# Kernel tuning notes

Measured on AMD Instinct MI355X. Metric: run time of the kernel, lower is better.

Reference implementation:

```python
import jax, jax.numpy as jnp
import numpy as np

N = 100000   # nodes
E = 1000000  # edges
F = 64       # in_features == out_features
ALPHA = 0.2  # leaky-relu negative slope


def setup_inputs() -> dict:
    key = jax.random.key(0)
    k = jax.random.split(key, 6)
    h = jax.random.normal(k[0], (N, F), jnp.float32)
    W = jax.random.normal(k[1], (F, F), jnp.float32) * 0.1   # Linear weight [out,in]
    Wb = jnp.zeros((F,), jnp.float32)
    a = jax.random.normal(k[2], (2 * F,), jnp.float32) * 0.1  # attn vector (Linear(2F,1))
    ab = jnp.zeros((), jnp.float32)
    src = jax.random.randint(k[3], (E,), 0, N, dtype=jnp.int32)
    dst = jax.random.randint(k[4], (E,), 0, N, dtype=jnp.int32)
    return {"h": h, "W": W, "Wb": Wb, "a": a, "ab": ab, "src": src, "dst": dst}


def reference(h, W, Wb, a, ab, src, dst):
    # Wh = W(h)  (dropout is identity in eval mode / dropout=0)
    Wh = h @ W.T + Wb                                   # [N, F]
    # e = leakyrelu(a([Wh_src || Wh_dst])) ; split a to avoid concat
    a_src, a_dst = a[:F], a[F:]
    e = jax.nn.leaky_relu(Wh[src] @ a_src + Wh[dst] @ a_dst + ab, ALPHA)  # [E]
    # segment softmax over destination nodes (DGL mailbox softmax)
    m = jax.ops.segment_max(e, dst, num_segments=N)     # [N], -inf for empty
    m = jnp.where(jnp.isfinite(m), m, 0.0)
    ex = jnp.exp(e - m[dst])                            # [E]
    denom = jax.ops.segment_sum(ex, dst, num_segments=N)
    attn = ex / jnp.where(denom[dst] > 0, denom[dst], 1.0)
    # weighted scatter-sum of source features to destinations
    h_prime = jax.ops.segment_sum(attn[:, None] * Wh[src], dst, num_segments=N)  # [N, F]
    return h_prime
```

## Files before the change

### kernel.cpp

```cpp
#include <hip/hip_runtime.h>

#define NF 64
#define ALPHA 0.2f
#define BSH 7
#define BNODES 128
#define CAPG 2048
#define PB 4096
#define HB 800
#define NBIN 1024

typedef unsigned int  uint;
typedef unsigned short ushort;

typedef __attribute__((ext_vector_type(8))) short  short8;
typedef __attribute__((ext_vector_type(4))) float  floatx4;

__device__ __forceinline__ ushort f2bf(float x) {
    uint u = __float_as_uint(x);
    u += 0x7fffu + ((u >> 16) & 1u);
    return (ushort)(u >> 16);
}

__device__ __forceinline__ short8 pack8(float4 lo, float4 hi) {
    short8 r;
    r[0] = (short)f2bf(lo.x); r[1] = (short)f2bf(lo.y);
    r[2] = (short)f2bf(lo.z); r[3] = (short)f2bf(lo.w);
    r[4] = (short)f2bf(hi.x); r[5] = (short)f2bf(hi.y);
    r[6] = (short)f2bf(hi.z); r[7] = (short)f2bf(hi.w);
    return r;
}

__global__ __launch_bounds__(256) void wh_part_kernel(
    const float* __restrict__ h, const float* __restrict__ W,
    const float* __restrict__ Wb, const float* __restrict__ a,
    ushort* __restrict__ whbf, float* __restrict__ s_src, float* __restrict__ s_dst,
    const int* __restrict__ src, const int* __restrict__ dst,
    int* __restrict__ bctr, uint* __restrict__ tmp,
    int N, int E, int edgeB, int NB)
{
    __shared__ uint   stage[PB];
    __shared__ ushort bid[PB];
    __shared__ int    hist[HB];
    __shared__ int    lbase[HB];
    __shared__ int    ctr[HB];
    __shared__ int    gbase[HB];
    __shared__ int    sw[256];

    int t = threadIdx.x;

    if ((int)blockIdx.x < edgeB) {
        int base = (int)blockIdx.x * PB;
        int total = E - base; if (total > PB) total = PB; if (total < 0) total = 0;

        for (int i = t; i < HB; i += 256) hist[i] = 0;
        __syncthreads();

        uint pk[16]; int bb[16];
        #pragma unroll
        for (int g = 0; g < 4; ++g) {
            int ei = base + g * 1024 + t * 4;
            int s4[4], d4[4];
            if (ei + 3 < E) {
                int4 sv = *(const int4*)&src[ei];
                int4 dv = *(const int4*)&dst[ei];
                s4[0]=sv.x; s4[1]=sv.y; s4[2]=sv.z; s4[3]=sv.w;
                d4[0]=dv.x; d4[1]=dv.y; d4[2]=dv.z; d4[3]=dv.w;
            } else {
                #pragma unroll
                for (int j = 0; j < 4; ++j) {
                    int e = ei + j;
                    s4[j] = (e < E) ? src[e] : -1;
                    d4[j] = (e < E) ? dst[e] : -1;
                }
            }
            #pragma unroll
            for (int j = 0; j < 4; ++j) {
                int i16 = g * 4 + j;
                if (d4[j] >= 0) {
                    pk[i16] = ((uint)s4[j] << BSH) | (uint)(d4[j] & (BNODES - 1));
                    bb[i16] = d4[j] >> BSH;
                    atomicAdd(&hist[bb[i16]], 1);
                } else bb[i16] = -1;
            }
        }
        __syncthreads();

        int b0 = t * 4;
        int c0 = 0, c1 = 0, c2 = 0, c3 = 0;
        if (b0 < HB)     c0 = hist[b0];
        if (b0 + 1 < HB) c1 = hist[b0+1];
        if (b0 + 2 < HB) c2 = hist[b0+2];
        if (b0 + 3 < HB) c3 = hist[b0+3];
        int tsum = c0 + c1 + c2 + c3;
        sw[t] = tsum; __syncthreads();
        for (int off = 1; off < 256; off <<= 1) {
            int x = (t >= off) ? sw[t - off] : 0;
            __syncthreads();
            sw[t] += x;
            __syncthreads();
        }
        int ex = sw[t] - tsum;
        if (b0 < HB)     { lbase[b0]   = ex; ex += c0; }
        if (b0 + 1 < HB) { lbase[b0+1] = ex; ex += c1; }
        if (b0 + 2 < HB) { lbase[b0+2] = ex; ex += c2; }
        if (b0 + 3 < HB) { lbase[b0+3] = ex; }
        __syncthreads();

        for (int q = t; q < NB; q += 256) {
            int c = hist[q];
            gbase[q] = c ? atomicAdd(&bctr[q], c) : 0;
            ctr[q] = lbase[q];
        }
        __syncthreads();

        #pragma unroll
        for (int i = 0; i < 16; ++i) {
            if (bb[i] >= 0) {
                int pos = atomicAdd(&ctr[bb[i]], 1);
                stage[pos] = pk[i];
                bid[pos] = (ushort)bb[i];
            }
        }
        __syncthreads();

        for (int i = t; i < total; i += 256) {
            int q = bid[i];
            int off = gbase[q] + (i - lbase[q]);
            if (off < CAPG) tmp[(size_t)q * CAPG + off] = stage[i];
        }
        return;
    }

    int lane = t & 63;
    int wave = t >> 6;
    int r0   = ((int)blockIdx.x - edgeB) * 256 + wave * 64;
    if (r0 >= N) return;
    int m    = lane & 15;
    int quad = lane >> 4;

    short8 bfrag[4][2];
    #pragma unroll
    for (int ct = 0; ct < 4; ++ct) {
        const float* wrow = W + (size_t)(ct * 16 + m) * 64 + quad * 8;
        #pragma unroll
        for (int kh = 0; kh < 2; ++kh) {
            float4 lo = *(const float4*)(wrow + kh * 32);
            float4 hi = *(const float4*)(wrow + kh * 32 + 4);
            bfrag[ct][kh] = pack8(lo, hi);
        }
    }

    float wb4[4], av1_4[4], av2_4[4];
    #pragma unroll
    for (int ct = 0; ct < 4; ++ct) {
        int col = ct * 16 + m;
        wb4[ct]   = Wb[col];
        av1_4[ct] = a[col];
        av2_4[ct] = a[64 + col];
    }

    for (int batch = 0; batch < 4; ++batch) {
        int rb = r0 + batch * 16;
        if (rb >= N) break;

        int row_a = rb + m; if (row_a >= N) row_a = N - 1;
        const float* hrow = h + (size_t)row_a * 64 + quad * 8;
        floatx4 zero = {0.f, 0.f, 0.f, 0.f};
        floatx4 acc[4] = {zero, zero, zero, zero};
        #pragma unroll
        for (int kh = 0; kh < 2; ++kh) {
            float4 lo = *(const float4*)(hrow + kh * 32);
            float4 hi = *(const float4*)(hrow + kh * 32 + 4);
            short8 af = pack8(lo, hi);
            #pragma unroll
            for (int ct = 0; ct < 4; ++ct)
                acc[ct] = __builtin_amdgcn_mfma_f32_16x16x32_bf16(af, bfrag[ct][kh], acc[ct], 0, 0, 0);
        }

        float p1[4] = {0.f, 0.f, 0.f, 0.f}, p2[4] = {0.f, 0.f, 0.f, 0.f};
        #pragma unroll
        for (int ct = 0; ct < 4; ++ct) {
            int col = ct * 16 + m;
            #pragma unroll
            for (int reg = 0; reg < 4; ++reg) {
                int row = rb + quad * 4 + reg;
                float v = acc[ct][reg] + wb4[ct];
                if (row < N) whbf[(size_t)row * 64 + col] = f2bf(v);
                p1[reg] += v * av1_4[ct];
                p2[reg] += v * av2_4[ct];
            }
        }
        #pragma unroll
        for (int off = 8; off >= 1; off >>= 1) {
            #pragma unroll
            for (int reg = 0; reg < 4; ++reg) {
                p1[reg] += __shfl_down(p1[reg], off, 16);
                p2[reg] += __shfl_down(p2[reg], off, 16);
            }
        }
        if (m == 0) {
            #pragma unroll
            for (int reg = 0; reg < 4; ++reg) {
                int row = rb + quad * 4 + reg;
                if (row < N) { s_src[row] = p1[reg]; s_dst[row] = p2[reg]; }
            }
        }
    }
}

#define STOREROW(node_, f_, dn_)                                          \
    if ((node_) < nlim) {                                                 \
        float inv_ = (dn_) > 0.f ? 1.f / (dn_) : 1.f;                     \
        float* orow_ = out + (size_t)(n0 + (node_)) * 64 + l8 * 8;        \
        float4 o0_, o1_;                                                  \
        o0_.x = f_[0]*inv_; o0_.y = f_[1]*inv_;                           \
        o0_.z = f_[2]*inv_; o0_.w = f_[3]*inv_;                           \
        o1_.x = f_[4]*inv_; o1_.y = f_[5]*inv_;                           \
        o1_.z = f_[6]*inv_; o1_.w = f_[7]*inv_;                           \
        *(float4*)orow_       = o0_;                                      \
        *(float4*)(orow_ + 4) = o1_;                                      \
    }

__global__ __launch_bounds__(512) void bucket_aggregate(
    const uint* __restrict__ tmp, const int* __restrict__ bctr,
    const float* __restrict__ s_src, const float* __restrict__ s_dst,
    const float* __restrict__ ab, const ushort* __restrict__ whbf,
    float* __restrict__ out, int N)
{
    __shared__ uint   ssrc[CAPG];
    __shared__ float  sexv[CAPG];
    __shared__ int    cnts[NBIN];
    __shared__ int    excl[NBIN + 1];
    __shared__ int    ctr[NBIN];
    __shared__ float  sdl[BNODES];
    __shared__ int    chist[64];
    __shared__ ushort rk[BNODES];

    int t = threadIdx.x;
    int b = blockIdx.x;
    int n0 = b << BSH;
    int cnt = bctr[b]; if (cnt > CAPG) cnt = CAPG;
    float ab0 = ab[0];

    for (int i = t; i < NBIN; i += 512) cnts[i] = 0;
    if (t < BNODES) {
        sdl[t] = (n0 + t < N) ? s_dst[n0 + t] + ab0 : 0.f;
    }
    if (t >= BNODES && t < BNODES + 64) chist[t - BNODES] = 0;
    __syncthreads();

    uint held[4]; int nh = 0;
    #pragma unroll
    for (int j = 0; j < 4; ++j) {
        int idx = t + j * 512;
        if (idx < cnt) {
            uint v = tmp[(size_t)b * CAPG + idx];
            held[nh++] = v;
            int bin = ((v & (BNODES - 1)) << 3) | ((v >> 21) & 7);
            atomicAdd(&cnts[bin], 1);
        }
    }
    __syncthreads();

    if (t < 64) {
        int base16 = t * 16;
        int c[16]; int s = 0;
        #pragma unroll
        for (int k = 0; k < 16; ++k) { c[k] = cnts[base16 + k]; s += c[k]; }
        int incl = s;
        #pragma unroll
        for (int off = 1; off < 64; off <<= 1) {
            int x = __shfl_up(incl, off, 64);
            if (t >= off) incl += x;
        }
        int e = incl - s;
        #pragma unroll
        for (int k = 0; k < 16; ++k) { excl[base16 + k] = e; ctr[base16 + k] = e; e += c[k]; }
        if (t == 63) excl[NBIN] = e;
    }
    __syncthreads();

    int myCnt = 0;
    if (t < BNODES) {
        myCnt = excl[(t << 3) + 8] - excl[t << 3];
        atomicAdd(&chist[myCnt > 63 ? 63 : myCnt], 1);
    }

    #pragma unroll
    for (int j = 0; j < 4; ++j) {
        if (j < nh) {
            uint v = held[j];
            uint s = v >> BSH;
            int node = v & (BNODES - 1);
            float e = s_src[s] + sdl[node];
            e = e > 0.f ? e : ALPHA * e;
            float ex = __expf(e);
            int bin = (node << 3) | ((v >> 21) & 7);
            int pos = atomicAdd(&ctr[bin], 1);
            ssrc[pos] = s; sexv[pos] = ex;
        }
    }
    __syncthreads();

    if (t < 64) {
        int c = chist[t];
        int incl = c;
        #pragma unroll
        for (int off = 1; off < 64; off <<= 1) {
            int x = __shfl_up(incl, off, 64);
            if (t >= off) incl += x;
        }
        chist[t] = incl - c;
    }
    __syncthreads();
    if (t < BNODES) {
        int r = atomicAdd(&chist[myCnt > 63 ? 63 : myCnt], 1);
        rk[r] = (ushort)t;
    }
    __syncthreads();

    int g = t >> 3, l8 = t & 7;
    int nlim = N - n0; if (nlim > BNODES) nlim = BNODES;
    int nodeP = rk[127 - g];
    int nodeQ = rk[g];

    int p0 = excl[nodeP << 3], nP = excl[(nodeP << 3) + 8] - p0;
    int q0 = excl[nodeQ << 3], nQ = excl[(nodeQ << 3) + 8] - q0;
    int total = nP + nQ;

    float f[8] = {0.f,0.f,0.f,0.f,0.f,0.f,0.f,0.f};
    float dn = 0.f;
    bool pDone = false;

    if (total > 0) {
        int i0 = (0 < nP) ? p0 : q0;
        float eC = sexv[i0];
        uint  sC = ssrc[i0];
        uint4 pC = ((const uint4*)(whbf + (size_t)sC * 64))[l8];

        for (int i = 0; i < total; ++i) {
            int nx = i + 1;
            int ix = (nx < total) ? ((nx < nP) ? p0 + nx : q0 + nx - nP) : 0;
            uint  sN = ssrc[ix];
            float eN = sexv[ix];
            uint4 pN = ((const uint4*)(whbf + (size_t)sN * 64))[l8];

            if (!pDone && i == nP) {
                STOREROW(nodeP, f, dn);
                #pragma unroll
                for (int k = 0; k < 8; ++k) f[k] = 0.f;
                dn = 0.f;
                pDone = true;
            }

            f[0] += eC * __uint_as_float(pC.x << 16);
            f[1] += eC * __uint_as_float(pC.x & 0xffff0000u);
            f[2] += eC * __uint_as_float(pC.y << 16);
            f[3] += eC * __uint_as_float(pC.y & 0xffff0000u);
            f[4] += eC * __uint_as_float(pC.z << 16);
            f[5] += eC * __uint_as_float(pC.z & 0xffff0000u);
            f[6] += eC * __uint_as_float(pC.w << 16);
            f[7] += eC * __uint_as_float(pC.w & 0xffff0000u);
            dn += eC;

            eC = eN; pC = pN;
        }
    }

    if (!pDone) {
        STOREROW(nodeP, f, dn);
        #pragma unroll
        for (int k = 0; k < 8; ++k) f[k] = 0.f;
        dn = 0.f;
    }
    STOREROW(nodeQ, f, dn);
}

extern "C" void kernel_launch(void* const* d_in, const int* in_sizes, int n_in,
                              void* d_out, int out_size, void* d_ws, size_t ws_size,
                              hipStream_t stream) {
    const float* h   = (const float*)d_in[0];
    const float* W   = (const float*)d_in[1];
    const float* Wb  = (const float*)d_in[2];
    const float* a   = (const float*)d_in[3];
    const float* ab  = (const float*)d_in[4];
    const int*   src = (const int*)d_in[5];
    const int*   dst = (const int*)d_in[6];

    int N = in_sizes[0] / NF;
    int E = in_sizes[5];
    float* out = (float*)d_out;
    int NB = (N + BNODES - 1) >> BSH;

    ushort* whbf   = (ushort*)d_ws;
    float*  s_src  = (float*)(whbf + (size_t)N * NF);
    float*  s_dst  = s_src + N;
    int*    bctr   = (int*)(s_dst + N);
    uint*   tmp    = (uint*)(bctr + NB);

    hipMemsetAsync(bctr, 0, (size_t)NB * sizeof(int), stream);

    int whB   = (N + 255) / 256;
    int edgeB = (E + PB - 1) / PB;

    wh_part_kernel<<<edgeB + whB, 256, 0, stream>>>(
        h, W, Wb, a, whbf, s_src, s_dst, src, dst, bctr, tmp, N, E, edgeB, NB);

    bucket_aggregate<<<NB, 512, 0, stream>>>(tmp, bctr, s_src, s_dst, ab, whbf, out, N);
}
```

Baseline: 131.1 us.

## Halve partition block size and split paired-node aggregation into two loops

```diff
diff --git a/kernel.cpp b/kernel.cpp
--- a/kernel.cpp
+++ b/kernel.cpp
@@ -5,7 +5,7 @@
 #define BSH 7
 #define BNODES 128
 #define CAPG 2048
-#define PB 4096
+#define PB 2048
 #define HB 800
 #define NBIN 1024
 
@@ -55,9 +55,9 @@
         for (int i = t; i < HB; i += 256) hist[i] = 0;
         __syncthreads();
 
-        uint pk[16]; int bb[16];
-        #pragma unroll
-        for (int g = 0; g < 4; ++g) {
+        uint pk[PB / 256]; int bb[PB / 256];
+        #pragma unroll
+        for (int g = 0; g < PB / 1024; ++g) {
             int ei = base + g * 1024 + t * 4;
             int s4[4], d4[4];
             if (ei + 3 < E) {
@@ -114,7 +114,7 @@
         __syncthreads();
 
         #pragma unroll
-        for (int i = 0; i < 16; ++i) {
+        for (int i = 0; i < PB / 256; ++i) {
             if (bb[i] >= 0) {
                 int pos = atomicAdd(&ctr[bb[i]], 1);
                 stage[pos] = pk[i];
@@ -207,6 +207,16 @@
         }
     }
 }
+
+#define ACC8(f_, e_, p_)                                    \
+    f_[0] += (e_) * __uint_as_float((p_).x << 16);          \
+    f_[1] += (e_) * __uint_as_float((p_).x & 0xffff0000u);  \
+    f_[2] += (e_) * __uint_as_float((p_).y << 16);          \
+    f_[3] += (e_) * __uint_as_float((p_).y & 0xffff0000u);  \
+    f_[4] += (e_) * __uint_as_float((p_).z << 16);          \
+    f_[5] += (e_) * __uint_as_float((p_).z & 0xffff0000u);  \
+    f_[6] += (e_) * __uint_as_float((p_).w << 16);          \
+    f_[7] += (e_) * __uint_as_float((p_).w & 0xffff0000u);
 
 #define STOREROW(node_, f_, dn_)                                          \
     if ((node_) < nlim) {                                                 \
@@ -326,52 +336,41 @@
 
     int p0 = excl[nodeP << 3], nP = excl[(nodeP << 3) + 8] - p0;
     int q0 = excl[nodeQ << 3], nQ = excl[(nodeQ << 3) + 8] - q0;
-    int total = nP + nQ;
 
     float f[8] = {0.f,0.f,0.f,0.f,0.f,0.f,0.f,0.f};
     float dn = 0.f;
-    bool pDone = false;
-
-    if (total > 0) {
-        int i0 = (0 < nP) ? p0 : q0;
-        float eC = sexv[i0];
-        uint  sC = ssrc[i0];
+
+    if (nP > 0) {
+        uint  sC = ssrc[p0];
+        float eC = sexv[p0];
         uint4 pC = ((const uint4*)(whbf + (size_t)sC * 64))[l8];
-
-        for (int i = 0; i < total; ++i) {
-            int nx = i + 1;
-            int ix = (nx < total) ? ((nx < nP) ? p0 + nx : q0 + nx - nP) : 0;
+        for (int i = 1; i <= nP; ++i) {
+            int ix = (i < nP) ? p0 + i : p0;
             uint  sN = ssrc[ix];
             float eN = sexv[ix];
             uint4 pN = ((const uint4*)(whbf + (size_t)sN * 64))[l8];
-
-            if (!pDone && i == nP) {
-                STOREROW(nodeP, f, dn);
-                #pragma unroll
-                for (int k = 0; k < 8; ++k) f[k] = 0.f;
-                dn = 0.f;
-                pDone = true;
-            }
-
-            f[0] += eC * __uint_as_float(pC.x << 16);
-            f[1] += eC * __uint_as_float(pC.x & 0xffff0000u);
-            f[2] += eC * __uint_as_float(pC.y << 16);
-            f[3] += eC * __uint_as_float(pC.y & 0xffff0000u);
-            f[4] += eC * __uint_as_float(pC.z << 16);
-            f[5] += eC * __uint_as_float(pC.z & 0xffff0000u);
-            f[6] += eC * __uint_as_float(pC.w << 16);
-            f[7] += eC * __uint_as_float(pC.w & 0xffff0000u);
-            dn += eC;
-
+            ACC8(f, eC, pC); dn += eC;
             eC = eN; pC = pN;
         }
     }
-
-    if (!pDone) {
-        STOREROW(nodeP, f, dn);
-        #pragma unroll
-        for (int k = 0; k < 8; ++k) f[k] = 0.f;
-        dn = 0.f;
+    STOREROW(nodeP, f, dn);
+
+    #pragma unroll
+    for (int k = 0; k < 8; ++k) f[k] = 0.f;
+    dn = 0.f;
+
+    if (nQ > 0) {
+        uint  sC = ssrc[q0];
+        float eC = sexv[q0];
+        uint4 pC = ((const uint4*)(whbf + (size_t)sC * 64))[l8];
+        for (int i = 1; i <= nQ; ++i) {
+            int ix = (i < nQ) ? q0 + i : q0;
+            uint  sN = ssrc[ix];
+            float eN = sexv[ix];
+            uint4 pN = ((const uint4*)(whbf + (size_t)sN * 64))[l8];
+            ACC8(f, eC, pC); dn += eC;
+            eC = eN; pC = pN;
+        }
     }
     STOREROW(nodeQ, f, dn);
 }
```

Result: slower. 149.3 us (+13.9%).
